# Performance work log

Measured on AMD Instinct MI355X. Metric: run time of the kernel, lower is better.

Reference implementation:

```python
import jax, jax.numpy as jnp
import numpy as np

N_NODES = 50000
N_EDGES = 800000
F_IN = 128
HIDDEN = 128
N_CLASSES = 40


def setup_inputs() -> dict:
    key = jax.random.key(0)
    k1, k2, k3, k4 = jax.random.split(key, 4)
    features = jax.random.normal(k1, (N_NODES, F_IN), dtype=jnp.float32)
    edge_index = jax.random.randint(k2, (2, N_EDGES), 0, N_NODES, dtype=jnp.int64)
    # Glorot-style init for the GCNConv linear weights, zero bias (PyG default)
    W1 = jax.random.normal(k3, (F_IN, HIDDEN), dtype=jnp.float32) * (1.0 / np.sqrt(F_IN))
    b1 = jnp.zeros((HIDDEN,), dtype=jnp.float32)
    W2 = jax.random.normal(k4, (HIDDEN, N_CLASSES), dtype=jnp.float32) * (1.0 / np.sqrt(HIDDEN))
    b2 = jnp.zeros((N_CLASSES,), dtype=jnp.float32)
    return {"features": features, "edge_index": edge_index,
            "W1": W1, "b1": b1, "W2": W2, "b2": b2}


def _gcn_norm(edge_index, num_nodes):
    # Add self-loops and compute symmetric normalization D^-1/2 (A+I) D^-1/2
    loop = jnp.arange(num_nodes, dtype=edge_index.dtype)
    src = jnp.concatenate([edge_index[0], loop])  # [E+N]
    dst = jnp.concatenate([edge_index[1], loop])  # [E+N]
    w = jnp.ones(src.shape[0], dtype=jnp.float32)
    deg = jax.ops.segment_sum(w, dst, num_segments=num_nodes)  # [N]
    dinv = jnp.where(deg > 0, jax.lax.rsqrt(deg), 0.0)
    norm = dinv[src] * w * dinv[dst]  # [E+N]
    return src, dst, norm


def _gcn_conv(x, W, b, src, dst, norm, num_nodes):
    h = x @ W  # linear transform first (PyG GCNConv): [N, out]
    msg = h[src] * norm[:, None]  # gather + scale: [E+N, out]
    out = jax.ops.segment_sum(msg, dst, num_segments=num_nodes)  # scatter-add
    return out + b


def reference(features, edge_index, W1, b1, W2, b2):
    n = features.shape[0]
    src, dst, norm = _gcn_norm(edge_index, n)
    x = jax.nn.relu(_gcn_conv(features, W1, b1, src, dst, norm, n))
    # dropout is identity at eval time (training=False)
    x = _gcn_conv(x, W2, b2, src, dst, norm, n)
    return jax.nn.log_softmax(x, axis=1)
```

## Files before the change

### kernel.cpp

```cpp
#include <hip/hip_runtime.h>
#include <hip/hip_bf16.h>
#include <math.h>

#define N_NODES 50000
#define N_EDGES 800000

#define SCAN_CHUNK 512
#define SCAN_NB ((N_NODES + SCAN_CHUNK - 1) / SCAN_CHUNK)

__global__ __launch_bounds__(256) void count_kernel(const int* __restrict__ ei,
                                                    int* __restrict__ cnt) {
  int e = blockIdx.x * 256 + threadIdx.x;
  if (e < N_EDGES) {
    int d = ei[N_EDGES + e];
    d = min(max(d, 0), N_NODES - 1);
    atomicAdd(&cnt[d], 1);
  }
}

__global__ __launch_bounds__(256) void scan_reduce(const int* __restrict__ cnt,
                                                   int* __restrict__ bsum) {
  __shared__ int s[256];
  int t = threadIdx.x;
  int i0 = blockIdx.x * SCAN_CHUNK + t * 2;
  int v = 0;
  if (i0 < N_NODES) v += cnt[i0];
  if (i0 + 1 < N_NODES) v += cnt[i0 + 1];
  s[t] = v;
  __syncthreads();
  for (int off = 128; off > 0; off >>= 1) {
    if (t < off) s[t] += s[t + off];
    __syncthreads();
  }
  if (t == 0) bsum[blockIdx.x] = s[0];
}

__global__ void scan_block(int* bsum) {
  __shared__ int s[128];
  int t = threadIdx.x;
  int v = (t < SCAN_NB) ? bsum[t] : 0;
  s[t] = v;
  __syncthreads();
  for (int off = 1; off < 128; off <<= 1) {
    int a = (t >= off) ? s[t - off] : 0;
    __syncthreads();
    s[t] += a;
    __syncthreads();
  }
  if (t < SCAN_NB) bsum[t] = s[t] - v;
}

__global__ __launch_bounds__(256) void scan_final(const int* __restrict__ cnt,
                                                  const int* __restrict__ bsum,
                                                  int* __restrict__ rowptr,
                                                  int* __restrict__ cursor,
                                                  float* __restrict__ dinv) {
  __shared__ int s[256];
  int t = threadIdx.x;
  int b = blockIdx.x;
  int i0 = b * SCAN_CHUNK + t * 2;
  int c0 = (i0 < N_NODES) ? cnt[i0] : 0;
  int c1 = (i0 + 1 < N_NODES) ? cnt[i0 + 1] : 0;
  int v = c0 + c1;
  s[t] = v;
  __syncthreads();
  for (int off = 1; off < 256; off <<= 1) {
    int a = (t >= off) ? s[t - off] : 0;
    __syncthreads();
    s[t] += a;
    __syncthreads();
  }
  int excl = s[t] - v + bsum[b];
  if (i0 < N_NODES) {
    rowptr[i0] = excl;
    cursor[i0] = excl;
    dinv[i0] = rsqrtf((float)(c0 + 1));
  }
  if (i0 + 1 < N_NODES) {
    rowptr[i0 + 1] = excl + c0;
    cursor[i0 + 1] = excl + c0;
    dinv[i0 + 1] = rsqrtf((float)(c1 + 1));
  }
  if (b == 0 && t == 0) rowptr[N_NODES] = N_EDGES;
}

__global__ __launch_bounds__(256) void fill_kernel(const int* __restrict__ ei,
                                                   int* __restrict__ cursor,
                                                   int* __restrict__ col) {
  int e = blockIdx.x * 256 + threadIdx.x;
  if (e >= N_EDGES) return;
  int srcv = ei[e];
  int dstv = ei[N_EDGES + e];
  srcv = min(max(srcv, 0), N_NODES - 1);
  dstv = min(max(dstv, 0), N_NODES - 1);
  int p = atomicAdd(&cursor[dstv], 1);
  col[p] = srcv;
}

__global__ __launch_bounds__(256) void gemm1_kernel(const float* __restrict__ X,
                                                    const float* __restrict__ W,
                                                    const float* __restrict__ dinv,
                                                    float* __restrict__ h1p) {
  __shared__ float xs[128 * 128];
  __shared__ float ws[128 * 128];
  int t = threadIdx.x;
  int row0 = blockIdx.x * 128;
#pragma unroll
  for (int it = 0; it < 16; ++it) {
    int idx = t + it * 256;
    int r = idx >> 5, kq = idx & 31;
    int gr = row0 + r;
    if (gr >= N_NODES) gr = N_NODES - 1;
    float4 v = *(const float4*)(X + (size_t)gr * 128 + kq * 4);
    *(float4*)(xs + r * 128 + ((kq ^ (r & 7)) << 2)) = v;
  }
#pragma unroll
  for (int it = 0; it < 16; ++it) {
    int idx = t + it * 256;
    int k = idx >> 5, jq = idx & 31;
    float4 v = *(const float4*)(W + k * 128 + jq * 4);
    int kc = k >> 2, kr = k & 3;
    int j0 = jq * 4;
    ws[(j0 + 0) * 128 + (((kc ^ ((j0 + 0) & 7)) << 2) | kr)] = v.x;
    ws[(j0 + 1) * 128 + (((kc ^ ((j0 + 1) & 7)) << 2) | kr)] = v.y;
    ws[(j0 + 2) * 128 + (((kc ^ ((j0 + 2) & 7)) << 2) | kr)] = v.z;
    ws[(j0 + 3) * 128 + (((kc ^ ((j0 + 3) & 7)) << 2) | kr)] = v.w;
  }
  __syncthreads();
  int wv = t >> 6, lane = t & 63;
  int wr = (wv >> 1) << 6, wc = (wv & 1) << 6;
  int tr = lane >> 3, tc = lane & 7;
  float acc[8][8];
#pragma unroll
  for (int i = 0; i < 8; ++i)
#pragma unroll
    for (int m = 0; m < 8; ++m) acc[i][m] = 0.f;
  for (int kq = 0; kq < 32; ++kq) {
    float4 xv[8], wvv[8];
#pragma unroll
    for (int i = 0; i < 8; ++i)
      xv[i] = *(const float4*)(xs + (wr + tr + 8 * i) * 128 + ((kq ^ tr) << 2));
#pragma unroll
    for (int m = 0; m < 8; ++m)
      wvv[m] = *(const float4*)(ws + (wc + tc + 8 * m) * 128 + ((kq ^ tc) << 2));
#pragma unroll
    for (int i = 0; i < 8; ++i)
#pragma unroll
      for (int m = 0; m < 8; ++m) {
        acc[i][m] = fmaf(xv[i].x, wvv[m].x, acc[i][m]);
        acc[i][m] = fmaf(xv[i].y, wvv[m].y, acc[i][m]);
        acc[i][m] = fmaf(xv[i].z, wvv[m].z, acc[i][m]);
        acc[i][m] = fmaf(xv[i].w, wvv[m].w, acc[i][m]);
      }
  }
#pragma unroll
  for (int i = 0; i < 8; ++i) {
    int gr = row0 + wr + tr + 8 * i;
    if (gr < N_NODES) {
      float di = dinv[gr];
#pragma unroll
      for (int m = 0; m < 8; ++m)
        h1p[(size_t)gr * 128 + wc + tc + 8 * m] = di * acc[i][m];
    }
  }
}

__global__ __launch_bounds__(256) void agg1_kernel(const float* __restrict__ h1p,
                                                   const int* __restrict__ rowptr,
                                                   const int* __restrict__ col,
                                                   const float* __restrict__ dinv,
                                                   const float* __restrict__ b1,
                                                   float* __restrict__ x2) {
  int wid = (blockIdx.x * 256 + threadIdx.x) >> 6;
  int lane = threadIdx.x & 63;
  if (wid >= N_NODES) return;
  int rs = rowptr[wid], re = rowptr[wid + 1];
  int f = lane * 2;
  const float2* hp2 = (const float2*)h1p;
  float2 acc = hp2[(size_t)wid * 64 + lane];
  for (int base = rs; base < re; base += 64) {
    int idx = base + lane;
    int c = (idx < re) ? col[idx] : 0;
    int nb = min(64, re - base);
    int e = 0;
    for (; e + 4 <= nb; e += 4) {
      int s0 = __shfl(c, e), s1 = __shfl(c, e + 1);
      int s2 = __shfl(c, e + 2), s3 = __shfl(c, e + 3);
      float2 v0 = hp2[(size_t)s0 * 64 + lane];
      float2 v1 = hp2[(size_t)s1 * 64 + lane];
      float2 v2 = hp2[(size_t)s2 * 64 + lane];
      float2 v3 = hp2[(size_t)s3 * 64 + lane];
      acc.x += (v0.x + v1.x) + (v2.x + v3.x);
      acc.y += (v0.y + v1.y) + (v2.y + v3.y);
    }
    for (; e < nb; ++e) {
      int s0 = __shfl(c, e);
      float2 v0 = hp2[(size_t)s0 * 64 + lane];
      acc.x += v0.x;
      acc.y += v0.y;
    }
  }
  float di = dinv[wid];
  float2 o;
  o.x = fmaxf(fmaf(di, acc.x, b1[f]), 0.f);
  o.y = fmaxf(fmaf(di, acc.y, b1[f + 1]), 0.f);
  *(float2*)(x2 + (size_t)wid * 128 + f) = o;
}

__global__ __launch_bounds__(256) void gemm2_kernel(const float* __restrict__ X2,
                                                    const float* __restrict__ W2,
                                                    const float* __restrict__ dinv,
                                                    float* __restrict__ h2p) {
  __shared__ float xs[64 * 128];
  __shared__ float ws[40 * 128];
  int t = threadIdx.x;
  int row0 = blockIdx.x * 64;
#pragma unroll
  for (int it = 0; it < 8; ++it) {
    int idx = t + it * 256;
    int r = idx >> 5, kq = idx & 31;
    int gr = row0 + r;
    if (gr >= N_NODES) gr = N_NODES - 1;
    float4 v = *(const float4*)(X2 + (size_t)gr * 128 + kq * 4);
    *(float4*)(xs + r * 128 + ((kq ^ (r & 7)) << 2)) = v;
  }
  for (int idx = t; idx < 1280; idx += 256) {
    int k = idx / 10, jq = idx % 10;
    float4 v = *(const float4*)(W2 + k * 40 + jq * 4);
    int kc = k >> 2, kr = k & 3;
    int j0 = jq * 4;
    ws[(j0 + 0) * 128 + (((kc ^ ((j0 + 0) & 7)) << 2) | kr)] = v.x;
    ws[(j0 + 1) * 128 + (((kc ^ ((j0 + 1) & 7)) << 2) | kr)] = v.y;
    ws[(j0 + 2) * 128 + (((kc ^ ((j0 + 2) & 7)) << 2) | kr)] = v.z;
    ws[(j0 + 3) * 128 + (((kc ^ ((j0 + 3) & 7)) << 2) | kr)] = v.w;
  }
  __syncthreads();
  int wv = t >> 6, lane = t & 63;
  int tr = lane >> 3, tc = lane & 7;
  int rbase = wv * 16;
  float acc[2][5];
#pragma unroll
  for (int i = 0; i < 2; ++i)
#pragma unroll
    for (int m = 0; m < 5; ++m) acc[i][m] = 0.f;
  for (int kq = 0; kq < 32; ++kq) {
    float4 xv[2], wvv[5];
#pragma unroll
    for (int i = 0; i < 2; ++i)
      xv[i] = *(const float4*)(xs + (rbase + tr + 8 * i) * 128 + ((kq ^ tr) << 2));
#pragma unroll
    for (int m = 0; m < 5; ++m)
      wvv[m] = *(const float4*)(ws + (tc + 8 * m) * 128 + ((kq ^ tc) << 2));
#pragma unroll
    for (int i = 0; i < 2; ++i)
#pragma unroll
      for (int m = 0; m < 5; ++m) {
        acc[i][m] = fmaf(xv[i].x, wvv[m].x, acc[i][m]);
        acc[i][m] = fmaf(xv[i].y, wvv[m].y, acc[i][m]);
        acc[i][m] = fmaf(xv[i].z, wvv[m].z, acc[i][m]);
        acc[i][m] = fmaf(xv[i].w, wvv[m].w, acc[i][m]);
      }
  }
#pragma unroll
  for (int i = 0; i < 2; ++i) {
    int gr = row0 + rbase + tr + 8 * i;
    if (gr < N_NODES) {
      float di = dinv[gr];
#pragma unroll
      for (int m = 0; m < 5; ++m)
        h2p[(size_t)gr * 40 + tc + 8 * m] = di * acc[i][m];
    }
  }
}

__global__ __launch_bounds__(256) void agg2_softmax_kernel(const float* __restrict__ h2p,
                                                           const int* __restrict__ rowptr,
                                                           const int* __restrict__ col,
                                                           const float* __restrict__ dinv,
                                                           const float* __restrict__ b2,
                                                           float* __restrict__ out) {
  int wid = (blockIdx.x * 256 + threadIdx.x) >> 6;
  int lane = threadIdx.x & 63;
  if (wid >= N_NODES) return;
  int rs = rowptr[wid], re = rowptr[wid + 1];
  bool act = lane < 40;
  float acc = act ? h2p[(size_t)wid * 40 + lane] : 0.f;
  for (int base = rs; base < re; base += 64) {
    int idx = base + lane;
    int c = (idx < re) ? col[idx] : 0;
    int nb = min(64, re - base);
    int e = 0;
    for (; e + 4 <= nb; e += 4) {
      int s0 = __shfl(c, e), s1 = __shfl(c, e + 1);
      int s2 = __shfl(c, e + 2), s3 = __shfl(c, e + 3);
      if (act) {
        float v0 = h2p[(size_t)s0 * 40 + lane];
        float v1 = h2p[(size_t)s1 * 40 + lane];
        float v2 = h2p[(size_t)s2 * 40 + lane];
        float v3 = h2p[(size_t)s3 * 40 + lane];
        acc += (v0 + v1) + (v2 + v3);
      }
    }
    for (; e < nb; ++e) {
      int s0 = __shfl(c, e);
      if (act) acc += h2p[(size_t)s0 * 40 + lane];
    }
  }
  float v = act ? fmaf(dinv[wid], acc, b2[lane]) : -1e30f;
  float m = v;
#pragma unroll
  for (int off = 32; off > 0; off >>= 1) m = fmaxf(m, __shfl_xor(m, off));
  float ex = act ? expf(v - m) : 0.f;
  float ssum = ex;
#pragma unroll
  for (int off = 32; off > 0; off >>= 1) ssum += __shfl_xor(ssum, off);
  float ls = logf(ssum);
  if (act) out[(size_t)wid * 40 + lane] = v - m - ls;
}

extern "C" void kernel_launch(void* const* d_in, const int* in_sizes, int n_in,
                              void* d_out, int out_size, void* d_ws, size_t ws_size,
                              hipStream_t stream) {
  const float* X = (const float*)d_in[0];
  const int* ei = (const int*)d_in[1];
  const float* W1 = (const float*)d_in[2];
  const float* b1 = (const float*)d_in[3];
  const float* W2 = (const float*)d_in[4];
  const float* b2 = (const float*)d_in[5];
  float* out = (float*)d_out;

  char* p = (char*)d_ws;
  auto carve = [&](size_t bytes) -> void* {
    void* q = (void*)p;
    p += (bytes + 255) & ~(size_t)255;
    return q;
  };
  float* h1p = (float*)carve((size_t)N_NODES * 128 * 4);
  float* x2 = (float*)carve((size_t)N_NODES * 128 * 4);
  float* h2p = (float*)carve((size_t)N_NODES * 40 * 4);
  int* col = (int*)carve((size_t)N_EDGES * 4);
  int* cnt = (int*)carve((size_t)N_NODES * 4);
  int* rowptr = (int*)carve((size_t)(N_NODES + 1) * 4);
  int* cursor = (int*)carve((size_t)N_NODES * 4);
  float* dinv = (float*)carve((size_t)N_NODES * 4);
  int* bsum = (int*)carve((size_t)SCAN_NB * 4);

  hipMemsetAsync(cnt, 0, (size_t)N_NODES * 4, stream);
  count_kernel<<<(N_EDGES + 255) / 256, 256, 0, stream>>>(ei, cnt);
  scan_reduce<<<SCAN_NB, 256, 0, stream>>>(cnt, bsum);
  scan_block<<<1, 128, 0, stream>>>(bsum);
  scan_final<<<SCAN_NB, 256, 0, stream>>>(cnt, bsum, rowptr, cursor, dinv);
  fill_kernel<<<(N_EDGES + 255) / 256, 256, 0, stream>>>(ei, cursor, col);
  gemm1_kernel<<<(N_NODES + 127) / 128, 256, 0, stream>>>(X, W1, dinv, h1p);
  agg1_kernel<<<(N_NODES + 3) / 4, 256, 0, stream>>>(h1p, rowptr, col, dinv, b1, x2);
  gemm2_kernel<<<(N_NODES + 63) / 64, 256, 0, stream>>>(x2, W2, dinv, h2p);
  agg2_softmax_kernel<<<(N_NODES + 3) / 4, 256, 0, stream>>>(h2p, rowptr, col, dinv, b2, out);
}
```

Measured before the change: 319.3 us.

## Split GEMM1 K into halves and widen agg1 gathers to float4 half-waves

```diff
diff --git a/kernel.cpp b/kernel.cpp
--- a/kernel.cpp
+++ b/kernel.cpp
@@ -101,32 +101,10 @@
                                                     const float* __restrict__ W,
                                                     const float* __restrict__ dinv,
                                                     float* __restrict__ h1p) {
-  __shared__ float xs[128 * 128];
-  __shared__ float ws[128 * 128];
+  __shared__ float xs[128 * 64];
+  __shared__ float ws[128 * 64];
   int t = threadIdx.x;
   int row0 = blockIdx.x * 128;
-#pragma unroll
-  for (int it = 0; it < 16; ++it) {
-    int idx = t + it * 256;
-    int r = idx >> 5, kq = idx & 31;
-    int gr = row0 + r;
-    if (gr >= N_NODES) gr = N_NODES - 1;
-    float4 v = *(const float4*)(X + (size_t)gr * 128 + kq * 4);
-    *(float4*)(xs + r * 128 + ((kq ^ (r & 7)) << 2)) = v;
-  }
-#pragma unroll
-  for (int it = 0; it < 16; ++it) {
-    int idx = t + it * 256;
-    int k = idx >> 5, jq = idx & 31;
-    float4 v = *(const float4*)(W + k * 128 + jq * 4);
-    int kc = k >> 2, kr = k & 3;
-    int j0 = jq * 4;
-    ws[(j0 + 0) * 128 + (((kc ^ ((j0 + 0) & 7)) << 2) | kr)] = v.x;
-    ws[(j0 + 1) * 128 + (((kc ^ ((j0 + 1) & 7)) << 2) | kr)] = v.y;
-    ws[(j0 + 2) * 128 + (((kc ^ ((j0 + 2) & 7)) << 2) | kr)] = v.z;
-    ws[(j0 + 3) * 128 + (((kc ^ ((j0 + 3) & 7)) << 2) | kr)] = v.w;
-  }
-  __syncthreads();
   int wv = t >> 6, lane = t & 63;
   int wr = (wv >> 1) << 6, wc = (wv & 1) << 6;
   int tr = lane >> 3, tc = lane & 7;
@@ -135,23 +113,49 @@
   for (int i = 0; i < 8; ++i)
 #pragma unroll
     for (int m = 0; m < 8; ++m) acc[i][m] = 0.f;
-  for (int kq = 0; kq < 32; ++kq) {
-    float4 xv[8], wvv[8];
-#pragma unroll
-    for (int i = 0; i < 8; ++i)
-      xv[i] = *(const float4*)(xs + (wr + tr + 8 * i) * 128 + ((kq ^ tr) << 2));
-#pragma unroll
-    for (int m = 0; m < 8; ++m)
-      wvv[m] = *(const float4*)(ws + (wc + tc + 8 * m) * 128 + ((kq ^ tc) << 2));
-#pragma unroll
-    for (int i = 0; i < 8; ++i)
-#pragma unroll
-      for (int m = 0; m < 8; ++m) {
-        acc[i][m] = fmaf(xv[i].x, wvv[m].x, acc[i][m]);
-        acc[i][m] = fmaf(xv[i].y, wvv[m].y, acc[i][m]);
-        acc[i][m] = fmaf(xv[i].z, wvv[m].z, acc[i][m]);
-        acc[i][m] = fmaf(xv[i].w, wvv[m].w, acc[i][m]);
-      }
+
+  for (int h = 0; h < 2; ++h) {
+    if (h) __syncthreads();
+#pragma unroll
+    for (int it = 0; it < 8; ++it) {
+      int idx = t + it * 256;
+      int r = idx >> 4, kq = idx & 15;
+      int gr = row0 + r;
+      if (gr >= N_NODES) gr = N_NODES - 1;
+      float4 v = *(const float4*)(X + (size_t)gr * 128 + h * 64 + kq * 4);
+      *(float4*)(xs + r * 64 + ((kq ^ (r & 7)) << 2)) = v;
+    }
+#pragma unroll
+    for (int it = 0; it < 8; ++it) {
+      int idx = t + it * 256;
+      int k = idx >> 5, jq = idx & 31;
+      float4 v = *(const float4*)(W + (size_t)(h * 64 + k) * 128 + jq * 4);
+      int kc = k >> 2, kr = k & 3;
+      int j0 = jq * 4;
+      ws[(j0 + 0) * 64 + (((kc ^ ((j0 + 0) & 7)) << 2) | kr)] = v.x;
+      ws[(j0 + 1) * 64 + (((kc ^ ((j0 + 1) & 7)) << 2) | kr)] = v.y;
+      ws[(j0 + 2) * 64 + (((kc ^ ((j0 + 2) & 7)) << 2) | kr)] = v.z;
+      ws[(j0 + 3) * 64 + (((kc ^ ((j0 + 3) & 7)) << 2) | kr)] = v.w;
+    }
+    __syncthreads();
+    for (int kq = 0; kq < 16; ++kq) {
+      float4 xv[8], wvv[8];
+#pragma unroll
+      for (int i = 0; i < 8; ++i)
+        xv[i] = *(const float4*)(xs + (wr + tr + 8 * i) * 64 + ((kq ^ tr) << 2));
+#pragma unroll
+      for (int m = 0; m < 8; ++m)
+        wvv[m] = *(const float4*)(ws + (wc + tc + 8 * m) * 64 + ((kq ^ tc) << 2));
+#pragma unroll
+      for (int i = 0; i < 8; ++i)
+#pragma unroll
+        for (int m = 0; m < 8; ++m) {
+          acc[i][m] = fmaf(xv[i].x, wvv[m].x, acc[i][m]);
+          acc[i][m] = fmaf(xv[i].y, wvv[m].y, acc[i][m]);
+          acc[i][m] = fmaf(xv[i].z, wvv[m].z, acc[i][m]);
+          acc[i][m] = fmaf(xv[i].w, wvv[m].w, acc[i][m]);
+        }
+    }
   }
 #pragma unroll
   for (int i = 0; i < 8; ++i) {
@@ -175,36 +179,63 @@
   int lane = threadIdx.x & 63;
   if (wid >= N_NODES) return;
   int rs = rowptr[wid], re = rowptr[wid + 1];
-  int f = lane * 2;
-  const float2* hp2 = (const float2*)h1p;
-  float2 acc = hp2[(size_t)wid * 64 + lane];
+  int half = lane >> 5;
+  int fl = lane & 31;
+  const float4* hp4 = (const float4*)h1p;
+  float4 z = {0.f, 0.f, 0.f, 0.f};
+  float4 a0 = (half == 0) ? hp4[(size_t)wid * 32 + fl] : z;
+  float4 a1 = z, a2 = z, a3 = z;
   for (int base = rs; base < re; base += 64) {
     int idx = base + lane;
     int c = (idx < re) ? col[idx] : 0;
     int nb = min(64, re - base);
     int e = 0;
-    for (; e + 4 <= nb; e += 4) {
-      int s0 = __shfl(c, e), s1 = __shfl(c, e + 1);
-      int s2 = __shfl(c, e + 2), s3 = __shfl(c, e + 3);
-      float2 v0 = hp2[(size_t)s0 * 64 + lane];
-      float2 v1 = hp2[(size_t)s1 * 64 + lane];
-      float2 v2 = hp2[(size_t)s2 * 64 + lane];
-      float2 v3 = hp2[(size_t)s3 * 64 + lane];
-      acc.x += (v0.x + v1.x) + (v2.x + v3.x);
-      acc.y += (v0.y + v1.y) + (v2.y + v3.y);
-    }
-    for (; e < nb; ++e) {
+    for (; e + 8 <= nb; e += 8) {
+      int s0 = __shfl(c, e + half);
+      int s1 = __shfl(c, e + 2 + half);
+      int s2 = __shfl(c, e + 4 + half);
+      int s3 = __shfl(c, e + 6 + half);
+      float4 v0 = hp4[(size_t)s0 * 32 + fl];
+      float4 v1 = hp4[(size_t)s1 * 32 + fl];
+      float4 v2 = hp4[(size_t)s2 * 32 + fl];
+      float4 v3 = hp4[(size_t)s3 * 32 + fl];
+      a0.x += v0.x; a0.y += v0.y; a0.z += v0.z; a0.w += v0.w;
+      a1.x += v1.x; a1.y += v1.y; a1.z += v1.z; a1.w += v1.w;
+      a2.x += v2.x; a2.y += v2.y; a2.z += v2.z; a2.w += v2.w;
+      a3.x += v3.x; a3.y += v3.y; a3.z += v3.z; a3.w += v3.w;
+    }
+    for (; e + 2 <= nb; e += 2) {
+      int s0 = __shfl(c, e + half);
+      float4 v0 = hp4[(size_t)s0 * 32 + fl];
+      a0.x += v0.x; a0.y += v0.y; a0.z += v0.z; a0.w += v0.w;
+    }
+    if (e < nb) {
       int s0 = __shfl(c, e);
-      float2 v0 = hp2[(size_t)s0 * 64 + lane];
-      acc.x += v0.x;
-      acc.y += v0.y;
-    }
-  }
-  float di = dinv[wid];
-  float2 o;
-  o.x = fmaxf(fmaf(di, acc.x, b1[f]), 0.f);
-  o.y = fmaxf(fmaf(di, acc.y, b1[f + 1]), 0.f);
-  *(float2*)(x2 + (size_t)wid * 128 + f) = o;
+      if (half == 0) {
+        float4 v0 = hp4[(size_t)s0 * 32 + fl];
+        a0.x += v0.x; a0.y += v0.y; a0.z += v0.z; a0.w += v0.w;
+      }
+    }
+  }
+  float4 a;
+  a.x = (a0.x + a1.x) + (a2.x + a3.x);
+  a.y = (a0.y + a1.y) + (a2.y + a3.y);
+  a.z = (a0.z + a1.z) + (a2.z + a3.z);
+  a.w = (a0.w + a1.w) + (a2.w + a3.w);
+  a.x += __shfl_xor(a.x, 32);
+  a.y += __shfl_xor(a.y, 32);
+  a.z += __shfl_xor(a.z, 32);
+  a.w += __shfl_xor(a.w, 32);
+  if (half == 0) {
+    float di = dinv[wid];
+    float4 bb = ((const float4*)b1)[fl];
+    float4 o;
+    o.x = fmaxf(fmaf(di, a.x, bb.x), 0.f);
+    o.y = fmaxf(fmaf(di, a.y, bb.y), 0.f);
+    o.z = fmaxf(fmaf(di, a.z, bb.z), 0.f);
+    o.w = fmaxf(fmaf(di, a.w, bb.w), 0.f);
+    *(float4*)(x2 + (size_t)wid * 128 + fl * 4) = o;
+  }
 }
 
 __global__ __launch_bounds__(256) void gemm2_kernel(const float* __restrict__ X2,
@@ -284,7 +315,8 @@
   if (wid >= N_NODES) return;
   int rs = rowptr[wid], re = rowptr[wid + 1];
   bool act = lane < 40;
-  float acc = act ? h2p[(size_t)wid * 40 + lane] : 0.f;
+  float ac0 = act ? h2p[(size_t)wid * 40 + lane] : 0.f;
+  float ac1 = 0.f, ac2 = 0.f, ac3 = 0.f;
   for (int base = rs; base < re; base += 64) {
     int idx = base + lane;
     int c = (idx < re) ? col[idx] : 0;
@@ -294,18 +326,18 @@
       int s0 = __shfl(c, e), s1 = __shfl(c, e + 1);
       int s2 = __shfl(c, e + 2), s3 = __shfl(c, e + 3);
       if (act) {
-        float v0 = h2p[(size_t)s0 * 40 + lane];
-        float v1 = h2p[(size_t)s1 * 40 + lane];
-        float v2 = h2p[(size_t)s2 * 40 + lane];
-        float v3 = h2p[(size_t)s3 * 40 + lane];
-        acc += (v0 + v1) + (v2 + v3);
+        ac0 += h2p[(size_t)s0 * 40 + lane];
+        ac1 += h2p[(size_t)s1 * 40 + lane];
+        ac2 += h2p[(size_t)s2 * 40 + lane];
+        ac3 += h2p[(size_t)s3 * 40 + lane];
       }
     }
     for (; e < nb; ++e) {
       int s0 = __shfl(c, e);
-      if (act) acc += h2p[(size_t)s0 * 40 + lane];
-    }
-  }
+      if (act) ac0 += h2p[(size_t)s0 * 40 + lane];
+    }
+  }
+  float acc = (ac0 + ac1) + (ac2 + ac3);
   float v = act ? fmaf(dinv[wid], acc, b2[lane]) : -1e30f;
   float m = v;
 #pragma unroll
```

After: 314.4 us. About the same (-1.5%).
